# Optimization experiments

Hardware: AMD Instinct MI355X
Metric: run time of the kernel (lower is better)

## Reference

```python
import jax, jax.numpy as jnp
import numpy as np

D_MODEL = 768
N_HEAD = 12
D_FF = 3072
SEQ = 2048
BSZ = 4
EPS = 1e-5


def _linear_params(key, d_in, d_out):
    k1, k2 = jax.random.split(key)
    bound = 1.0 / np.sqrt(d_in)
    W = jax.random.uniform(k1, (d_in, d_out), jnp.float32, -bound, bound)
    b = jax.random.uniform(k2, (d_out,), jnp.float32, -bound, bound)
    return W, b


def setup_inputs() -> dict:
    key = jax.random.key(0)
    ks = jax.random.split(key, 8)
    src = jax.random.normal(ks[0], (SEQ, BSZ, D_MODEL), jnp.float32)
    Wq, bq = _linear_params(ks[1], D_MODEL, D_MODEL)
    Wk, bk = _linear_params(ks[2], D_MODEL, D_MODEL)
    Wv, bv = _linear_params(ks[3], D_MODEL, D_MODEL)
    Wo, bo = _linear_params(ks[4], D_MODEL, D_MODEL)
    W1, b1 = _linear_params(ks[5], D_MODEL, D_FF)
    W2, b2 = _linear_params(ks[6], D_FF, D_MODEL)
    g1 = jnp.ones((D_MODEL,), jnp.float32)
    be1 = jnp.zeros((D_MODEL,), jnp.float32)
    g2 = jnp.ones((D_MODEL,), jnp.float32)
    be2 = jnp.zeros((D_MODEL,), jnp.float32)
    return dict(src=src, Wq=Wq, bq=bq, Wk=Wk, bk=bk, Wv=Wv, bv=bv,
                Wo=Wo, bo=bo, W1=W1, b1=b1, W2=W2, b2=b2,
                g1=g1, be1=be1, g2=g2, be2=be2)


def _layer_norm(x, g, b):
    mu = jnp.mean(x, axis=-1, keepdims=True)
    var = jnp.mean(jnp.square(x - mu), axis=-1, keepdims=True)
    return (x - mu) * jax.lax.rsqrt(var + EPS) * g + b


def reference(src, Wq, bq, Wk, bk, Wv, bv, Wo, bo, W1, b1, W2, b2, g1, be1, g2, be2):
    L, B, D = src.shape
    H = N_HEAD
    hd = D // H
    # in-projection: (L,B,D) -> (B*H, L, hd)
    def split_heads(x):
        return x.reshape(L, B * H, hd).transpose(1, 0, 2)
    q = split_heads(src @ Wq + bq)
    k = split_heads(src @ Wk + bk)
    v = split_heads(src @ Wv + bv)
    # NOTE: original code applies NO 1/sqrt(head_dim) scaling
    scores = jnp.einsum('bqd,bkd->bqk', q, k)  # (B*H, L, L)
    attn = jax.nn.softmax(scores, axis=-1)
    attn_out = jnp.einsum('bqk,bkd->bqd', attn, v)  # (B*H, L, hd)
    # out-projection
    attn_out = attn_out.transpose(1, 0, 2).reshape(L, B, D)
    src2 = attn_out @ Wo + bo
    x = _layer_norm(src + src2, g1, be1)
    ff = jax.nn.gelu(x @ W1 + b1, approximate=False) @ W2 + b2
    return _layer_norm(x + ff, g2, be2)
```

## Files before the change

kernel.cpp:

```cpp
#include <hip/hip_runtime.h>
#include <math.h>

#define D_MODEL 768
#define N_HEAD  12
#define HD      64
#define D_FF    3072
#define SEQ     2048
#define BSZ     4
#define NROWS   (SEQ * BSZ)

typedef unsigned short u16;
typedef __attribute__((ext_vector_type(8))) short short8;
typedef __attribute__((ext_vector_type(4))) float float4v;

enum { FLAG_GELU = 1, FLAG_ABLK = 2, FLAG_CBBLK = 4 };

__device__ __forceinline__ float gelu_exact(float x) {
    return 0.5f * x * (1.0f + erff(x * 0.70710678118654752440f));
}
__device__ __forceinline__ u16 f2b(float f) {
    unsigned u = __builtin_bit_cast(unsigned, f);
    return (u16)((u + 0x7fffu + ((u >> 16) & 1u)) >> 16);
}
__device__ __forceinline__ float b2f(u16 x) {
    return __builtin_bit_cast(float, (unsigned)x << 16);
}
__device__ __forceinline__ void gll16(const u16* g, u16* l) {
    __builtin_amdgcn_global_load_lds(
        (const __attribute__((address_space(1))) unsigned*)g,
        (__attribute__((address_space(3))) unsigned*)l, 16, 0, 0);
}
__device__ __forceinline__ size_t blk_off(int row, int col, int k32) {
    return ((size_t)((row >> 7) * k32 + (col >> 5)) << 12)
         + ((row & 127) << 5) + (col & 31);
}

__global__ __launch_bounds__(256) void gemm_bt(
    const u16* __restrict__ A, int lda,
    const u16* __restrict__ Bt,
    const float* __restrict__ bias,
    const float* __restrict__ residf, const u16* __restrict__ residb, int ldr,
    float* __restrict__ Cf, u16* __restrict__ Cb, int ldc,
    int K, int flags)
{
    __shared__ u16 Ab[2][128 * 32];
    __shared__ u16 Bb[2][128 * 32];

    const int tid  = threadIdx.x;
    const int lane = tid & 63, wv = tid >> 6;
    const int row0 = blockIdx.x * 128, col0 = blockIdx.y * 128;
    const int mw = (wv & 1) * 64, nw = (wv >> 1) * 64;
    const int fr = lane & 15, fk = (lane >> 4) * 8;
    const int k32 = K >> 5;
    const int nIter = K >> 5;

    auto stage = [&](int buf, int k0) {
        const u16* baseB = Bt + (((size_t)(col0 >> 7) * k32 + (k0 >> 5)) << 12);
        if (flags & FLAG_ABLK) {
            const u16* baseA = A + (((size_t)(row0 >> 7) * k32 + (k0 >> 5)) << 12);
            #pragma unroll
            for (int i = 0; i < 2; ++i) {
                const int cid = i * 256 + wv * 64 + lane;
                gll16(baseA + (size_t)cid * 8, Ab[buf] + (size_t)cid * 8);
                gll16(baseB + (size_t)cid * 8, Bb[buf] + (size_t)cid * 8);
            }
        } else {
            #pragma unroll
            for (int i = 0; i < 2; ++i) {
                const int cid = i * 256 + wv * 64 + lane;
                const int r = cid >> 2, ch = (cid & 3) * 8;
                gll16(A + (size_t)(row0 + r) * lda + k0 + ch, Ab[buf] + (size_t)cid * 8);
                gll16(baseB + (size_t)cid * 8, Bb[buf] + (size_t)cid * 8);
            }
        }
    };

    float4v acc[4][4];
    #pragma unroll
    for (int i = 0; i < 4; ++i)
        #pragma unroll
        for (int j = 0; j < 4; ++j)
            acc[i][j] = float4v{0.f, 0.f, 0.f, 0.f};

    stage(0, 0);
    for (int it = 0; it < nIter; ++it) {
        const int cur = it & 1;
        __syncthreads();
        if (it + 1 < nIter) stage(cur ^ 1, (it + 1) * 32);

        short8 af[4], bfr[4];
        #pragma unroll
        for (int t = 0; t < 4; ++t) {
            af[t]  = *(const short8*)&Ab[cur][(mw + t * 16 + fr) * 32 + fk];
            bfr[t] = *(const short8*)&Bb[cur][(nw + t * 16 + fr) * 32 + fk];
        }
        #pragma unroll
        for (int mt = 0; mt < 4; ++mt)
            #pragma unroll
            for (int nt = 0; nt < 4; ++nt)
                acc[mt][nt] = __builtin_amdgcn_mfma_f32_16x16x32_bf16(
                    af[mt], bfr[nt], acc[mt][nt], 0, 0, 0);
    }

    #pragma unroll
    for (int mt = 0; mt < 4; ++mt)
        #pragma unroll
        for (int nt = 0; nt < 4; ++nt)
            #pragma unroll
            for (int r = 0; r < 4; ++r) {
                const int row = row0 + mw + mt * 16 + (lane >> 4) * 4 + r;
                const int col = col0 + nw + nt * 16 + fr;
                float v = acc[mt][nt][r];
                if (bias)              v += bias[col];
                if (flags & FLAG_GELU) v = gelu_exact(v);
                if (residf)            v += residf[(size_t)row * ldr + col];
                if (residb)            v += b2f(residb[blk_off(row, col, 24)]);
                if (Cf) Cf[(size_t)row * ldc + col] = v;
                if (Cb) Cb[(flags & FLAG_CBBLK) ? blk_off(row, col, ldc >> 5)
                                                : (size_t)row * ldc + col] = f2b(v);
            }
}

__global__ __launch_bounds__(256) void gemm_bt64(
    const u16* __restrict__ A, int lda,
    const u16* __restrict__ Bt,
    const float* __restrict__ bias,
    const float* __restrict__ residf, const u16* __restrict__ residb, int ldr,
    float* __restrict__ Cf, u16* __restrict__ Cb, int ldc,
    int K, int flags)
{
    __shared__ u16 Ab[2][128 * 32];
    __shared__ u16 Bb[2][64 * 32];

    const int tid  = threadIdx.x;
    const int lane = tid & 63, wv = tid >> 6;
    const int row0 = blockIdx.x * 128, col0 = blockIdx.y * 64;
    const int mw = wv * 32;
    const int fr = lane & 15, hi = lane >> 4, fk = hi * 8;
    const int k32 = K >> 5;
    const int nIter = K >> 5;

    auto stage = [&](int buf, int k0) {
        const u16* baseB = Bt + (((size_t)(col0 >> 7) * k32 + (k0 >> 5)) << 12)
                              + ((col0 & 64) << 5);
        gll16(baseB + (size_t)tid * 8, Bb[buf] + (size_t)tid * 8);
        if (flags & FLAG_ABLK) {
            const u16* baseA = A + (((size_t)(row0 >> 7) * k32 + (k0 >> 5)) << 12);
            #pragma unroll
            for (int i = 0; i < 2; ++i) {
                const int cid = i * 256 + tid;
                gll16(baseA + (size_t)cid * 8, Ab[buf] + (size_t)cid * 8);
            }
        } else {
            #pragma unroll
            for (int i = 0; i < 2; ++i) {
                const int cid = i * 256 + tid;
                const int r = cid >> 2, ch = (cid & 3) * 8;
                gll16(A + (size_t)(row0 + r) * lda + k0 + ch, Ab[buf] + (size_t)cid * 8);
            }
        }
    };

    float4v acc[2][4];
    #pragma unroll
    for (int i = 0; i < 2; ++i)
        #pragma unroll
        for (int j = 0; j < 4; ++j)
            acc[i][j] = float4v{0.f, 0.f, 0.f, 0.f};

    stage(0, 0);
    for (int it = 0; it < nIter; ++it) {
        const int cur = it & 1;
        __syncthreads();
        if (it + 1 < nIter) stage(cur ^ 1, (it + 1) * 32);

        short8 af[2], bfr[4];
        #pragma unroll
        for (int t = 0; t < 2; ++t)
            af[t] = *(const short8*)&Ab[cur][(mw + t * 16 + fr) * 32 + fk];
        #pragma unroll
        for (int t = 0; t < 4; ++t)
            bfr[t] = *(const short8*)&Bb[cur][(t * 16 + fr) * 32 + fk];
        #pragma unroll
        for (int mt = 0; mt < 2; ++mt)
            #pragma unroll
            for (int nt = 0; nt < 4; ++nt)
                acc[mt][nt] = __builtin_amdgcn_mfma_f32_16x16x32_bf16(
                    af[mt], bfr[nt], acc[mt][nt], 0, 0, 0);
    }

    #pragma unroll
    for (int mt = 0; mt < 2; ++mt)
        #pragma unroll
        for (int nt = 0; nt < 4; ++nt)
            #pragma unroll
            for (int r = 0; r < 4; ++r) {
                const int row = row0 + mw + mt * 16 + hi * 4 + r;
                const int col = col0 + nt * 16 + fr;
                float v = acc[mt][nt][r];
                if (bias)              v += bias[col];
                if (flags & FLAG_GELU) v = gelu_exact(v);
                if (residf)            v += residf[(size_t)row * ldr + col];
                if (residb)            v += b2f(residb[blk_off(row, col, 24)]);
                if (Cf) Cf[(size_t)row * ldc + col] = v;
                if (Cb) Cb[(flags & FLAG_CBBLK) ? blk_off(row, col, ldc >> 5)
                                                : (size_t)row * ldc + col] = f2b(v);
            }
}

__global__ __launch_bounds__(256) void vt_kernel(
    const u16* __restrict__ qkv, u16* __restrict__ vt)
{
    __shared__ u16 t[64][72];
    const int tid = threadIdx.x;
    const int bh = blockIdx.y, b = bh / N_HEAD, h = bh % N_HEAD;
    const int l0 = blockIdx.x * 64;
    #pragma unroll
    for (int p = 0; p < 2; ++p) {
        const int idx = p * 256 + tid;
        const int lr = idx >> 3, c8 = (idx & 7) * 8;
        *(short8*)&t[lr][c8] = *(const short8*)
            &qkv[blk_off((l0 + lr) * BSZ + b, 1536 + h * 64 + c8, 72)];
    }
    __syncthreads();
    #pragma unroll
    for (int p = 0; p < 2; ++p) {
        const int idx = p * 256 + tid;
        const int dr = idx >> 3, l8 = (idx & 7) * 8;
        short8 vv;
        #pragma unroll
        for (int j = 0; j < 8; ++j) vv[j] = (short)t[l8 + j][dr];
        *(short8*)&vt[((size_t)(bh * 64 + dr)) * SEQ + l0 + l8] = vv;
    }
}

__global__ __launch_bounds__(256) void attn_kernel(
    const u16* __restrict__ qkv, const u16* __restrict__ vt,
    u16* __restrict__ o)
{
    __shared__ u16 Kt[2][64 * 64];
    __shared__ u16 Vt[2][64 * 64];
    __shared__ u16 PQ[128 * 72];

    const int tid  = threadIdx.x;
    const int lane = tid & 63, wv = tid >> 6;
    const int fr = lane & 15, hi = lane >> 4;
    const int bh = blockIdx.x, b = bh / N_HEAD, h = bh % N_HEAD;
    const int q0 = blockIdx.y * 128;

    auto stageKV = [&](int buf, int kt) {
        #pragma unroll
        for (int i = 0; i < 2; ++i) {
            const int cid = i * 256 + wv * 64 + lane;
            const int r = cid >> 3, c = cid & 7;
            const int cs = (c ^ (r & 7)) * 8;
            gll16(qkv + blk_off((kt + r) * BSZ + b, 768 + h * 64 + cs, 72),
                  Kt[buf] + (size_t)cid * 8);
            gll16(vt + (size_t)(bh * 64 + r) * SEQ + kt + cs,
                  Vt[buf] + (size_t)cid * 8);
        }
    };

    #pragma unroll
    for (int i = 0; i < 4; ++i) {
        const int cid = i * 256 + wv * 64 + lane;
        const int r = cid >> 3, c = cid & 7;
        gll16(qkv + blk_off((q0 + r) * BSZ + b, h * 64 + ((c ^ (r & 7)) * 8), 72),
              PQ + (size_t)cid * 8);
    }
    stageKV(0, 0);
    __syncthreads();

    short8 qf[2][2];
    #pragma unroll
    for (int mt = 0; mt < 2; ++mt) {
        const int row = wv * 32 + mt * 16 + fr;
        #pragma unroll
        for (int kb = 0; kb < 2; ++kb)
            qf[mt][kb] = *(const short8*)&PQ[row * 64 + (((kb << 2) + hi) ^ (fr & 7)) * 8];
    }

    const short8 ones = {(short)0x3F80, (short)0x3F80, (short)0x3F80, (short)0x3F80,
                         (short)0x3F80, (short)0x3F80, (short)0x3F80, (short)0x3F80};
    float4v oacc[2][4], ls[2];
    #pragma unroll
    for (int mt = 0; mt < 2; ++mt) {
        ls[mt] = float4v{0.f, 0.f, 0.f, 0.f};
        #pragma unroll
        for (int nt = 0; nt < 4; ++nt) oacc[mt][nt] = float4v{0.f, 0.f, 0.f, 0.f};
    }

    for (int it = 0; it < SEQ / 64; ++it) {
        const int cur = it & 1;
        __syncthreads();
        if (it + 1 < SEQ / 64) stageKV(cur ^ 1, (it + 1) * 64);

        float4v s[2][4];
        #pragma unroll
        for (int mt = 0; mt < 2; ++mt)
            #pragma unroll
            for (int nt = 0; nt < 4; ++nt) s[mt][nt] = float4v{0.f, 0.f, 0.f, 0.f};
        #pragma unroll
        for (int kb = 0; kb < 2; ++kb) {
            short8 kfr[4];
            #pragma unroll
            for (int nt = 0; nt < 4; ++nt)
                kfr[nt] = *(const short8*)&Kt[cur][(nt * 16 + fr) * 64 + (((kb << 2) + hi) ^ (fr & 7)) * 8];
            #pragma unroll
            for (int mt = 0; mt < 2; ++mt)
                #pragma unroll
                for (int nt = 0; nt < 4; ++nt)
                    s[mt][nt] = __builtin_amdgcn_mfma_f32_16x16x32_bf16(
                        qf[mt][kb], kfr[nt], s[mt][nt], 0, 0, 0);
        }

        #pragma unroll
        for (int mt = 0; mt < 2; ++mt)
            #pragma unroll
            for (int nt = 0; nt < 4; ++nt)
                #pragma unroll
                for (int r = 0; r < 4; ++r)
                    PQ[(wv * 32 + mt * 16 + hi * 4 + r) * 72 + nt * 16 + fr]
                        = f2b(__expf(s[mt][nt][r] - 16.0f));

        #pragma unroll
        for (int kb = 0; kb < 2; ++kb) {
            short8 pf[2], vfr[4];
            #pragma unroll
            for (int mt = 0; mt < 2; ++mt)
                pf[mt] = *(const short8*)&PQ[(wv * 32 + mt * 16 + fr) * 72 + kb * 32 + hi * 8];
            #pragma unroll
            for (int nt = 0; nt < 4; ++nt)
                vfr[nt] = *(const short8*)&Vt[cur][(nt * 16 + fr) * 64 + (((kb << 2) + hi) ^ (fr & 7)) * 8];
            #pragma unroll
            for (int mt = 0; mt < 2; ++mt) {
                ls[mt] = __builtin_amdgcn_mfma_f32_16x16x32_bf16(pf[mt], ones, ls[mt], 0, 0, 0);
                #pragma unroll
                for (int nt = 0; nt < 4; ++nt)
                    oacc[mt][nt] = __builtin_amdgcn_mfma_f32_16x16x32_bf16(
                        pf[mt], vfr[nt], oacc[mt][nt], 0, 0, 0);
            }
        }
    }

    #pragma unroll
    for (int mt = 0; mt < 2; ++mt)
        #pragma unroll
        for (int r = 0; r < 4; ++r) {
            const int qr = wv * 32 + mt * 16 + hi * 4 + r;
            const float linv = 1.0f / ls[mt][r];
            #pragma unroll
            for (int nt = 0; nt < 4; ++nt)
                o[((size_t)(q0 + qr) * BSZ + b) * D_MODEL + h * 64 + nt * 16 + fr]
                    = f2b(oacc[mt][nt][r] * linv);
        }
}

__global__ __launch_bounds__(256) void ln_kernel(
    const float* __restrict__ x, float* __restrict__ outf, u16* __restrict__ outb,
    const float* __restrict__ g, const float* __restrict__ be)
{
    const int row = blockIdx.x;
    const int tid = threadIdx.x;
    const float* xr = x + (size_t)row * D_MODEL;
    float v[3];
    float s = 0.0f, sq = 0.0f;
    #pragma unroll
    for (int j = 0; j < 3; ++j) {
        v[j] = xr[tid + 256 * j];
        s  += v[j];
        sq += v[j] * v[j];
    }
    #pragma unroll
    for (int off = 32; off > 0; off >>= 1) {
        s  += __shfl_down(s, off);
        sq += __shfl_down(sq, off);
    }
    __shared__ float ws_[8], wq_[8];
    if ((tid & 63) == 0) { ws_[tid >> 6] = s; wq_[tid >> 6] = sq; }
    __syncthreads();
    if (tid == 0) {
        float S = 0.0f, Q = 0.0f;
        #pragma unroll
        for (int w = 0; w < 4; ++w) { S += ws_[w]; Q += wq_[w]; }
        ws_[4] = S; wq_[4] = Q;
    }
    __syncthreads();
    const float mu   = ws_[4] * (1.0f / D_MODEL);
    const float var  = wq_[4] * (1.0f / D_MODEL) - mu * mu;
    const float rstd = rsqrtf(var + 1e-5f);
    #pragma unroll
    for (int j = 0; j < 3; ++j) {
        const int c = tid + 256 * j;
        const float y = (v[j] - mu) * rstd * g[c] + be[c];
        if (outf) outf[(size_t)row * D_MODEL + c] = y;
        if (outb) outb[blk_off(row, c, 24)] = f2b(y);
    }
}

__global__ __launch_bounds__(256) void transpose_bf(
    const float* __restrict__ in, u16* __restrict__ out, int R, int Cn)
{
    __shared__ float t[32][33];
    const int c0 = blockIdx.x * 32, r0 = blockIdx.y * 32;
    const int tx = threadIdx.x & 31, ty = threadIdx.x >> 5;
    #pragma unroll
    for (int i = 0; i < 4; ++i)
        t[ty + i * 8][tx] = in[(size_t)(r0 + ty + i * 8) * Cn + c0 + tx];
    __syncthreads();
    const int k32 = R >> 5;
    #pragma unroll
    for (int i = 0; i < 4; ++i)
        out[blk_off(c0 + ty + i * 8, r0 + tx, k32)] = f2b(t[tx][ty + i * 8]);
}

__global__ __launch_bounds__(256) void conv_bf_blk(
    const float* __restrict__ in, u16* __restrict__ out)
{
    const int i = blockIdx.x * 256 + threadIdx.x;
    const int row = i / 96;
    const int c8  = (i - row * 96) * 8;
    const float4 a = *(const float4*)&in[(size_t)row * 768 + c8];
    const float4 b = *(const float4*)&in[(size_t)row * 768 + c8 + 4];
    uint4 pk;
    pk.x = (unsigned)f2b(a.x) | ((unsigned)f2b(a.y) << 16);
    pk.y = (unsigned)f2b(a.z) | ((unsigned)f2b(a.w) << 16);
    pk.z = (unsigned)f2b(b.x) | ((unsigned)f2b(b.y) << 16);
    pk.w = (unsigned)f2b(b.z) | ((unsigned)f2b(b.w) << 16);
    *(uint4*)&out[blk_off(row, c8, 24)] = pk;
}

__global__ __launch_bounds__(256) void pack_bias(
    const float* __restrict__ bq, const float* __restrict__ bk,
    const float* __restrict__ bv, float* __restrict__ dst)
{
    const int i = blockIdx.x * 256 + threadIdx.x;
    if (i < 2304)
        dst[i] = (i < 768) ? bq[i] : (i < 1536) ? bk[i - 768] : bv[i - 1536];
}

extern "C" void kernel_launch(void* const* d_in, const int* in_sizes, int n_in,
                              void* d_out, int out_size, void* d_ws, size_t ws_size,
                              hipStream_t stream)
{
    (void)in_sizes; (void)n_in; (void)out_size; (void)ws_size;
    const float* src = (const float*)d_in[0];
    const float* Wq  = (const float*)d_in[1];
    const float* bq  = (const float*)d_in[2];
    const float* Wk  = (const float*)d_in[3];
    const float* bk  = (const float*)d_in[4];
    const float* Wv  = (const float*)d_in[5];
    const float* bv  = (const float*)d_in[6];
    const float* Wo  = (const float*)d_in[7];
    const float* bo  = (const float*)d_in[8];
    const float* W1  = (const float*)d_in[9];
    const float* b1  = (const float*)d_in[10];
    const float* W2  = (const float*)d_in[11];
    const float* b2  = (const float*)d_in[12];
    const float* g1  = (const float*)d_in[13];
    const float* be1 = (const float*)d_in[14];
    const float* g2  = (const float*)d_in[15];
    const float* be2 = (const float*)d_in[16];
    float* out = (float*)d_out;

    char* w = (char*)d_ws;
    u16* WqkvT = (u16*)w; w += (size_t)2304 * 768 * 2;
    u16* WoT   = (u16*)w; w += (size_t)768 * 768 * 2;
    u16* W1T   = (u16*)w; w += (size_t)D_FF * 768 * 2;
    u16* W2T   = (u16*)w; w += (size_t)768 * D_FF * 2;
    float* bqkv = (float*)w; w += 2304 * 4 + 64;
    char* A0 = w; w += (size_t)NROWS * 768 * 2;
    char* A1 = w; w += (size_t)NROWS * 2304 * 2;
    char* A2 = w; w += (size_t)NROWS * 768 * 2;
    u16*   srcb  = (u16*)A0;
    u16*   vtb   = (u16*)A0;
    u16*   qkvb  = (u16*)A1;
    float* sum   = (float*)A1;
    u16*   attnb = (u16*)A2;
    u16*   x1b   = (u16*)A2;
    u16*   hb    = (u16*)A0;

    const dim3 blk(256);

    transpose_bf<<<dim3(24, 24), blk, 0, stream>>>(Wq, WqkvT,                 768, 768);
    transpose_bf<<<dim3(24, 24), blk, 0, stream>>>(Wk, WqkvT + 768 * 768,     768, 768);
    transpose_bf<<<dim3(24, 24), blk, 0, stream>>>(Wv, WqkvT + 2 * 768 * 768, 768, 768);
    transpose_bf<<<dim3(24, 24), blk, 0, stream>>>(Wo, WoT, 768, 768);
    transpose_bf<<<dim3(96, 24), blk, 0, stream>>>(W1, W1T, 768, 3072);
    transpose_bf<<<dim3(24, 96), blk, 0, stream>>>(W2, W2T, 3072, 768);
    pack_bias<<<dim3(9), blk, 0, stream>>>(bq, bk, bv, bqkv);
    conv_bf_blk<<<dim3(NROWS * 96 / 256), blk, 0, stream>>>(src, srcb);

    gemm_bt<<<dim3(64, 18), blk, 0, stream>>>(srcb, 0, WqkvT, bqkv,
        nullptr, nullptr, 0, nullptr, qkvb, 2304, 768, FLAG_ABLK | FLAG_CBBLK);

    vt_kernel<<<dim3(32, 48), blk, 0, stream>>>(qkvb, vtb);
    attn_kernel<<<dim3(BSZ * N_HEAD, SEQ / 128), blk, 0, stream>>>(qkvb, vtb, attnb);

    gemm_bt64<<<dim3(64, 12), blk, 0, stream>>>(attnb, 768, WoT, bo,
        src, nullptr, 768, sum, nullptr, 768, 768, 0);
    ln_kernel<<<NROWS, blk, 0, stream>>>(sum, nullptr, x1b, g1, be1);

    gemm_bt<<<dim3(64, 24), blk, 0, stream>>>(x1b, 0, W1T, b1,
        nullptr, nullptr, 0, nullptr, hb, 3072, 768, FLAG_GELU | FLAG_ABLK | FLAG_CBBLK);
    gemm_bt64<<<dim3(64, 12), blk, 0, stream>>>(hb, 0, W2T, b2,
        nullptr, x1b, 768, out, nullptr, 768, 3072, FLAG_ABLK);

    ln_kernel<<<NROWS, blk, 0, stream>>>(out, out, nullptr, g2, be2);
}
```

Before: 503.0 us.

## Fuse prep kernels, use one-wavefront-per-row layernorm, swizzle V transpose LDS

Merges the six weight-transpose launches, the bias pack and the source bf16 conversion into a single prep kernel that dispatches on block index, which removes launch overhead. Rewrites layernorm so each 64-lane wavefront owns one row, using float4 loads and a shuffle-xor reduction instead of shared memory and two block barriers. Adds an XOR swizzle to the V transpose shared tile to avoid LDS bank conflicts on the column reads. The prep kernel's block-index branching adds some divergence across block types, and the layernorm still uses the single-pass E[x^2]-mu^2 variance.

```diff
diff --git a/kernel.cpp b/kernel.cpp
--- a/kernel.cpp
+++ b/kernel.cpp
@@ -219,7 +219,8 @@
     for (int p = 0; p < 2; ++p) {
         const int idx = p * 256 + tid;
         const int lr = idx >> 3, c8 = (idx & 7) * 8;
-        *(short8*)&t[lr][c8] = *(const short8*)
+        const int ch = (idx & 7) ^ ((idx >> 6) & 7);
+        *(short8*)&t[lr][ch * 8] = *(const short8*)
             &qkv[blk_off((l0 + lr) * BSZ + b, 1536 + h * 64 + c8, 72)];
     }
     __syncthreads();
@@ -227,9 +228,10 @@
     for (int p = 0; p < 2; ++p) {
         const int idx = p * 256 + tid;
         const int dr = idx >> 3, l8 = (idx & 7) * 8;
+        const int sc = (((dr >> 3) ^ (idx & 7)) << 3) + (dr & 7);
         short8 vv;
         #pragma unroll
-        for (int j = 0; j < 8; ++j) vv[j] = (short)t[l8 + j][dr];
+        for (int j = 0; j < 8; ++j) vv[j] = (short)t[l8 + j][sc];
         *(short8*)&vt[((size_t)(bh * 64 + dr)) * SEQ + l0 + l8] = vv;
     }
 }
@@ -360,50 +362,51 @@
     const float* __restrict__ x, float* __restrict__ outf, u16* __restrict__ outb,
     const float* __restrict__ g, const float* __restrict__ be)
 {
-    const int row = blockIdx.x;
-    const int tid = threadIdx.x;
-    const float* xr = x + (size_t)row * D_MODEL;
-    float v[3];
-    float s = 0.0f, sq = 0.0f;
+    const int wv = threadIdx.x >> 6, lane = threadIdx.x & 63;
+    const int row = blockIdx.x * 4 + wv;
+    const float4* xr = (const float4*)(x + (size_t)row * D_MODEL);
+    float4 v[3];
+    float s = 0.f, sq = 0.f;
     #pragma unroll
     for (int j = 0; j < 3; ++j) {
-        v[j] = xr[tid + 256 * j];
-        s  += v[j];
-        sq += v[j] * v[j];
+        v[j] = xr[j * 64 + lane];
+        s  += v[j].x + v[j].y + v[j].z + v[j].w;
+        sq += v[j].x * v[j].x + v[j].y * v[j].y + v[j].z * v[j].z + v[j].w * v[j].w;
     }
     #pragma unroll
     for (int off = 32; off > 0; off >>= 1) {
-        s  += __shfl_down(s, off);
-        sq += __shfl_down(sq, off);
-    }
-    __shared__ float ws_[8], wq_[8];
-    if ((tid & 63) == 0) { ws_[tid >> 6] = s; wq_[tid >> 6] = sq; }
-    __syncthreads();
-    if (tid == 0) {
-        float S = 0.0f, Q = 0.0f;
-        #pragma unroll
-        for (int w = 0; w < 4; ++w) { S += ws_[w]; Q += wq_[w]; }
-        ws_[4] = S; wq_[4] = Q;
-    }
-    __syncthreads();
-    const float mu   = ws_[4] * (1.0f / D_MODEL);
-    const float var  = wq_[4] * (1.0f / D_MODEL) - mu * mu;
+        s  += __shfl_xor(s, off);
+        sq += __shfl_xor(sq, off);
+    }
+    const float mu   = s * (1.0f / D_MODEL);
+    const float var  = sq * (1.0f / D_MODEL) - mu * mu;
     const float rstd = rsqrtf(var + 1e-5f);
     #pragma unroll
     for (int j = 0; j < 3; ++j) {
-        const int c = tid + 256 * j;
-        const float y = (v[j] - mu) * rstd * g[c] + be[c];
-        if (outf) outf[(size_t)row * D_MODEL + c] = y;
-        if (outb) outb[blk_off(row, c, 24)] = f2b(y);
-    }
-}
-
-__global__ __launch_bounds__(256) void transpose_bf(
-    const float* __restrict__ in, u16* __restrict__ out, int R, int Cn)
-{
-    __shared__ float t[32][33];
-    const int c0 = blockIdx.x * 32, r0 = blockIdx.y * 32;
-    const int tx = threadIdx.x & 31, ty = threadIdx.x >> 5;
+        const int e4 = j * 64 + lane;
+        const float4 gv = ((const float4*)g)[e4];
+        const float4 bv = ((const float4*)be)[e4];
+        float4 y;
+        y.x = (v[j].x - mu) * rstd * gv.x + bv.x;
+        y.y = (v[j].y - mu) * rstd * gv.y + bv.y;
+        y.z = (v[j].z - mu) * rstd * gv.z + bv.z;
+        y.w = (v[j].w - mu) * rstd * gv.w + bv.w;
+        if (outf) ((float4*)(outf + (size_t)row * D_MODEL))[e4] = y;
+        if (outb) {
+            uint2 pk;
+            pk.x = (unsigned)f2b(y.x) | ((unsigned)f2b(y.y) << 16);
+            pk.y = (unsigned)f2b(y.z) | ((unsigned)f2b(y.w) << 16);
+            *(uint2*)&outb[blk_off(row, e4 * 4, 24)] = pk;
+        }
+    }
+}
+
+__device__ __forceinline__ void transpose_body(
+    const float* __restrict__ in, u16* __restrict__ out, int R, int Cn,
+    int bx, int by, int tid, float (*t)[33])
+{
+    const int c0 = bx * 32, r0 = by * 32;
+    const int tx = tid & 31, ty = tid >> 5;
     #pragma unroll
     for (int i = 0; i < 4; ++i)
         t[ty + i * 8][tx] = in[(size_t)(r0 + ty + i * 8) * Cn + c0 + tx];
@@ -414,29 +417,51 @@
         out[blk_off(c0 + ty + i * 8, r0 + tx, k32)] = f2b(t[tx][ty + i * 8]);
 }
 
-__global__ __launch_bounds__(256) void conv_bf_blk(
-    const float* __restrict__ in, u16* __restrict__ out)
-{
-    const int i = blockIdx.x * 256 + threadIdx.x;
-    const int row = i / 96;
-    const int c8  = (i - row * 96) * 8;
-    const float4 a = *(const float4*)&in[(size_t)row * 768 + c8];
-    const float4 b = *(const float4*)&in[(size_t)row * 768 + c8 + 4];
-    uint4 pk;
-    pk.x = (unsigned)f2b(a.x) | ((unsigned)f2b(a.y) << 16);
-    pk.y = (unsigned)f2b(a.z) | ((unsigned)f2b(a.w) << 16);
-    pk.z = (unsigned)f2b(b.x) | ((unsigned)f2b(b.y) << 16);
-    pk.w = (unsigned)f2b(b.z) | ((unsigned)f2b(b.w) << 16);
-    *(uint4*)&out[blk_off(row, c8, 24)] = pk;
-}
-
-__global__ __launch_bounds__(256) void pack_bias(
+__global__ __launch_bounds__(256) void prep_kernel(
+    const float* __restrict__ Wq, const float* __restrict__ Wk,
+    const float* __restrict__ Wv, const float* __restrict__ Wo,
+    const float* __restrict__ W1, const float* __restrict__ W2,
+    const float* __restrict__ src,
     const float* __restrict__ bq, const float* __restrict__ bk,
-    const float* __restrict__ bv, float* __restrict__ dst)
-{
-    const int i = blockIdx.x * 256 + threadIdx.x;
-    if (i < 2304)
-        dst[i] = (i < 768) ? bq[i] : (i < 1536) ? bk[i - 768] : bv[i - 1536];
+    const float* __restrict__ bv,
+    u16* __restrict__ WqkvT, u16* __restrict__ WoT,
+    u16* __restrict__ W1T, u16* __restrict__ W2T,
+    u16* __restrict__ srcb, float* __restrict__ bqkv)
+{
+    __shared__ float t[32][33];
+    const int id = blockIdx.x, tid = threadIdx.x;
+    if (id < 6912) {
+        const float* tin; u16* tout; int R, Cn, bx, by;
+        if (id < 2304) {
+            const int z = id / 576, i = id - z * 576;
+            tin  = (z == 0) ? Wq : (z == 1) ? Wk : (z == 2) ? Wv : Wo;
+            tout = (z == 3) ? WoT : WqkvT + z * 768 * 768;
+            R = 768; Cn = 768; bx = i % 24; by = i / 24;
+        } else if (id < 4608) {
+            const int i = id - 2304;
+            tin = W1; tout = W1T; R = 768; Cn = 3072; bx = i % 96; by = i / 96;
+        } else {
+            const int i = id - 4608;
+            tin = W2; tout = W2T; R = 3072; Cn = 768; bx = i % 24; by = i / 24;
+        }
+        transpose_body(tin, tout, R, Cn, bx, by, tid, t);
+    } else if (id < 9984) {
+        const int i = (id - 6912) * 256 + tid;
+        const int row = i / 96;
+        const int c8  = (i - row * 96) * 8;
+        const float4 a = *(const float4*)&src[(size_t)row * 768 + c8];
+        const float4 b = *(const float4*)&src[(size_t)row * 768 + c8 + 4];
+        uint4 pk;
+        pk.x = (unsigned)f2b(a.x) | ((unsigned)f2b(a.y) << 16);
+        pk.y = (unsigned)f2b(a.z) | ((unsigned)f2b(a.w) << 16);
+        pk.z = (unsigned)f2b(b.x) | ((unsigned)f2b(b.y) << 16);
+        pk.w = (unsigned)f2b(b.z) | ((unsigned)f2b(b.w) << 16);
+        *(uint4*)&srcb[blk_off(row, c8, 24)] = pk;
+    } else {
+        const int i = (id - 9984) * 256 + tid;
+        if (i < 2304)
+            bqkv[i] = (i < 768) ? bq[i] : (i < 1536) ? bk[i - 768] : bv[i - 1536];
+    }
 }
 
 extern "C" void kernel_launch(void* const* d_in, const int* in_sizes, int n_in,
@@ -482,14 +507,9 @@
 
     const dim3 blk(256);
 
-    transpose_bf<<<dim3(24, 24), blk, 0, stream>>>(Wq, WqkvT,                 768, 768);
-    transpose_bf<<<dim3(24, 24), blk, 0, stream>>>(Wk, WqkvT + 768 * 768,     768, 768);
-    transpose_bf<<<dim3(24, 24), blk, 0, stream>>>(Wv, WqkvT + 2 * 768 * 768, 768, 768);
-    transpose_bf<<<dim3(24, 24), blk, 0, stream>>>(Wo, WoT, 768, 768);
-    transpose_bf<<<dim3(96, 24), blk, 0, stream>>>(W1, W1T, 768, 3072);
-    transpose_bf<<<dim3(24, 96), blk, 0, stream>>>(W2, W2T, 3072, 768);
-    pack_bias<<<dim3(9), blk, 0, stream>>>(bq, bk, bv, bqkv);
-    conv_bf_blk<<<dim3(NROWS * 96 / 256), blk, 0, stream>>>(src, srcb);
+    prep_kernel<<<dim3(9993), blk, 0, stream>>>(
+        Wq, Wk, Wv, Wo, W1, W2, src, bq, bk, bv,
+        WqkvT, WoT, W1T, W2T, srcb, bqkv);
 
     gemm_bt<<<dim3(64, 18), blk, 0, stream>>>(srcb, 0, WqkvT, bqkv,
         nullptr, nullptr, 0, nullptr, qkvb, 2304, 768, FLAG_ABLK | FLAG_CBBLK);
@@ -499,12 +519,12 @@
 
     gemm_bt64<<<dim3(64, 12), blk, 0, stream>>>(attnb, 768, WoT, bo,
         src, nullptr, 768, sum, nullptr, 768, 768, 0);
-    ln_kernel<<<NROWS, blk, 0, stream>>>(sum, nullptr, x1b, g1, be1);
+    ln_kernel<<<dim3(NROWS / 4), blk, 0, stream>>>(sum, nullptr, x1b, g1, be1);
 
     gemm_bt<<<dim3(64, 24), blk, 0, stream>>>(x1b, 0, W1T, b1,
         nullptr, nullptr, 0, nullptr, hb, 3072, 768, FLAG_GELU | FLAG_ABLK | FLAG_CBBLK);
     gemm_bt64<<<dim3(64, 12), blk, 0, stream>>>(hb, 0, W2T, b2,
         nullptr, x1b, 768, out, nullptr, 768, 3072, FLAG_ABLK);
 
-    ln_kernel<<<NROWS, blk, 0, stream>>>(out, out, nullptr, g2, be2);
-}
+    ln_kernel<<<dim3(NROWS / 4), blk, 0, stream>>>(out, out, nullptr, g2, be2);
+}
```

Result: slower. 540.4 us (+7.4%).
